# Kernel tuning notes

Hardware: AMD Instinct MI355X
Metric: run time of the kernel (lower is better)

Reference implementation:

```python
import jax, jax.numpy as jnp
import numpy as np

NUM_E = 100000
NUM_R = 500
HIDDEN = 64
BATCH = 32
GAMMA = 12.0
EPSILON = 2.0
EMB_RANGE = (GAMMA + EPSILON) / HIDDEN  # 0.21875
PI = 3.141592653589793


def setup_inputs() -> dict:
    key = jax.random.key(0)
    k1, k2, k3 = jax.random.split(key, 3)
    facts = jax.random.randint(k1, (BATCH, 3), 0, 1000, dtype=jnp.int64)  # col0<num_e, col1<2*num_r
    entity_embedding = jax.random.uniform(
        k2, (NUM_E, 2 * HIDDEN), dtype=jnp.float32, minval=-EMB_RANGE, maxval=EMB_RANGE)
    relation_embedding = jax.random.uniform(
        k3, (NUM_R * 2, HIDDEN), dtype=jnp.float32, minval=-EMB_RANGE, maxval=EMB_RANGE)
    return {"facts": facts, "entity_embedding": entity_embedding,
            "relation_embedding": relation_embedding}


def reference(facts, entity_embedding, relation_embedding):
    # Gather head/relation embeddings for the batch
    head = entity_embedding[facts[:, 0]]          # [B, 2D]
    relation = relation_embedding[facts[:, 1]]    # [B, D]

    re_head, im_head = jnp.split(head, 2, axis=1)           # [B, D] each
    re_tail, im_tail = jnp.split(entity_embedding, 2, axis=1)  # [E, D] each

    phase = relation / (EMB_RANGE / PI)
    re_rel = jnp.cos(phase)
    im_rel = jnp.sin(phase)

    # Complex rotation of head by relation: [B, D]
    re_rot = re_head * re_rel - im_head * im_rel
    im_rot = re_head * im_rel + im_head * re_rel

    # Broadcast difference against all entities: [B, E, D]
    re_diff = re_rot[:, None, :] - re_tail[None, :, :]
    im_diff = im_rot[:, None, :] - im_tail[None, :, :]

    # Per-component complex modulus, summed over dim -> [B, E]
    dist = jnp.sqrt(re_diff * re_diff + im_diff * im_diff).sum(axis=2)
    return GAMMA - dist
```

## Files before the change

kernel.cpp:

```cpp
#include <hip/hip_runtime.h>
#include <math.h>

#define NUM_E   100000
#define GAMMA_F 12.0f
#define EMB_RANGE_F 0.21875f
#define INV_TWO_EMB (1.0f / (2.0f * EMB_RANGE_F))

#define TILE_E  16
#define NT      (NUM_E / TILE_E)
#define GRID    2048

typedef float v4f __attribute__((ext_vector_type(4)));
typedef float v2f __attribute__((ext_vector_type(2)));

static __device__ __forceinline__ v2f pk_sub(v2f a, v2f b) {
    v2f d;
    asm("v_pk_add_f32 %0, %1, %2 neg_lo:[0,1] neg_hi:[0,1]"
        : "=v"(d) : "v"(a), "v"(b));
    return d;
}
static __device__ __forceinline__ v2f pk_mul(v2f a, v2f b) {
    v2f d;
    asm("v_pk_mul_f32 %0, %1, %2" : "=v"(d) : "v"(a), "v"(b));
    return d;
}
static __device__ __forceinline__ v2f pk_fma(v2f a, v2f b, v2f c) {
    v2f d;
    asm("v_pk_fma_f32 %0, %1, %2, %3" : "=v"(d) : "v"(a), "v"(b), "v"(c));
    return d;
}
static __device__ __forceinline__ float sq2(v2f dx, v2f dy) {
    v2f sq = pk_fma(dy, dy, pk_mul(dx, dx));
    return __builtin_amdgcn_sqrtf(sq.x) + __builtin_amdgcn_sqrtf(sq.y);
}
static __device__ __forceinline__ v2f lo2(v4f v) { return __builtin_shufflevector(v, v, 0, 1); }
static __device__ __forceinline__ v2f hi2(v4f v) { return __builtin_shufflevector(v, v, 2, 3); }

template <int CTRL>
static __device__ __forceinline__ float dpp_xor_add(float x) {
    int y = __builtin_amdgcn_update_dpp(0, __float_as_int(x), CTRL, 0xF, 0xF, true);
    return x + __int_as_float(y);
}

static __device__ __forceinline__ float dist_entity(
        v4f er0, v4f er1, v4f ei0, v4f ei1,
        const v2f RR[4], const v2f RI[4]) {
    v2f e2[4] = { lo2(er0), hi2(er0), lo2(er1), hi2(er1) };
    v2f i2[4] = { lo2(ei0), hi2(ei0), lo2(ei1), hi2(ei1) };
    float s0 = sq2(pk_sub(RR[0], e2[0]), pk_sub(RI[0], i2[0]));
    float s1 = sq2(pk_sub(RR[1], e2[1]), pk_sub(RI[1], i2[1]));
    float s2 = sq2(pk_sub(RR[2], e2[2]), pk_sub(RI[2], i2[2]));
    float s3 = sq2(pk_sub(RR[3], e2[3]), pk_sub(RI[3], i2[3]));
    float v = (s0 + s1) + (s2 + s3);
    v = dpp_xor_add<0xB1>(v);
    v = dpp_xor_add<0x4E>(v);
    v = dpp_xor_add<0x141>(v);
    return GAMMA_F - v;
}

static __device__ __forceinline__ void stage_chunk(const float* g, float* l) {
    __builtin_amdgcn_global_load_lds(
        (const __attribute__((address_space(1))) void*)g,
        (__attribute__((address_space(3))) void*)l,
        16, 0, 0);
}

__global__ __launch_bounds__(256, 2) void rotate_dist_fused(
        const int*   __restrict__ facts,
        const float* __restrict__ ent,
        const float* __restrict__ rel,
        float*       __restrict__ out) {
    __shared__ __align__(16) float sbuf[2][TILE_E * 128];

    const int t    = threadIdx.x;
    const int lane = t & 63;
    const int wv   = t >> 6;
    const int bq   = lane >> 3;
    const int dg   = lane & 7;
    const int b    = wv * 8 + bq;

    int tile = blockIdx.x;

    {
        const float* g = ent + (size_t)tile * (TILE_E * 128) + wv * 512 + lane * 4;
        float* l = &sbuf[0][wv * 512];
        stage_chunk(g, l);
        stage_chunk(g + 256, l + 256);
    }

    v2f RR[4], RI[4];
    {
        const int f0 = facts[b * 3 + 0];
        const int f1 = facts[b * 3 + 1];
        const float* hp = ent + (size_t)f0 * 128 + dg * 8;
        const float* rp = rel + (size_t)f1 * 64  + dg * 8;
        v4f hre0 = *(const v4f*)(hp);
        v4f hre1 = *(const v4f*)(hp + 4);
        v4f him0 = *(const v4f*)(hp + 64);
        v4f him1 = *(const v4f*)(hp + 68);
        v4f ph0  = *(const v4f*)(rp);
        v4f ph1  = *(const v4f*)(rp + 4);
        v4f rr0, rr1, ri0, ri1;
#pragma unroll
        for (int j = 0; j < 4; ++j) {
            float rev0 = ph0[j] * INV_TWO_EMB;
            float s0 = __builtin_amdgcn_sinf(rev0);
            float c0 = __builtin_amdgcn_cosf(rev0);
            rr0[j] = hre0[j] * c0 - him0[j] * s0;
            ri0[j] = hre0[j] * s0 + him0[j] * c0;
            float rev1 = ph1[j] * INV_TWO_EMB;
            float s1 = __builtin_amdgcn_sinf(rev1);
            float c1 = __builtin_amdgcn_cosf(rev1);
            rr1[j] = hre1[j] * c1 - him1[j] * s1;
            ri1[j] = hre1[j] * s1 + him1[j] * c1;
        }
        RR[0] = lo2(rr0); RR[1] = hi2(rr0); RR[2] = lo2(rr1); RR[3] = hi2(rr1);
        RI[0] = lo2(ri0); RI[1] = hi2(ri0); RI[2] = lo2(ri1); RI[3] = hi2(ri1);
    }

    float* obase = out + (size_t)b * NUM_E;

    int cur = 0;
    __syncthreads();

    while (true) {
        const int nxt = tile + GRID;
        if (nxt < NT) {
            const float* g = ent + (size_t)nxt * (TILE_E * 128) + wv * 512 + lane * 4;
            float* l = &sbuf[cur ^ 1][wv * 512];
            stage_chunk(g, l);
            stage_chunk(g + 256, l + 256);
        }

        const float* csrc = &sbuf[cur][0];
        float* op = obase + tile * TILE_E;
#pragma unroll
        for (int q = 0; q < 4; ++q) {
            v4f vout;
#pragma unroll
            for (int i = 0; i < 4; ++i) {
                const float* ep = csrc + (q * 4 + i) * 128 + dg * 8;
                v4f er0 = *(const v4f*)(ep);
                v4f er1 = *(const v4f*)(ep + 4);
                v4f ei0 = *(const v4f*)(ep + 64);
                v4f ei1 = *(const v4f*)(ep + 68);
                vout[i] = dist_entity(er0, er1, ei0, ei1, RR, RI);
            }
            if (dg == q) *(v4f*)(op + q * 4) = vout;
        }

        if (nxt >= NT) break;
        __syncthreads();
        cur ^= 1;
        tile = nxt;
    }
}

extern "C" void kernel_launch(void* const* d_in, const int* in_sizes, int n_in,
                              void* d_out, int out_size, void* d_ws, size_t ws_size,
                              hipStream_t stream) {
    const int*   facts = (const int*)d_in[0];
    const float* ent   = (const float*)d_in[1];
    const float* rel   = (const float*)d_in[2];
    float*       out   = (float*)d_out;
    (void)d_ws; (void)ws_size;

    rotate_dist_fused<<<dim3(GRID), dim3(256), 0, stream>>>(facts, ent, rel, out);
}
```

Baseline: 116.5 us.

## Compute two batch rows per thread to reuse each LDS entity load

Each wave now handles 16 batch rows on half of the entity tile instead of 8 rows on the whole tile. Each thread keeps rotated head vectors for two batch rows and reuses every entity value it reads from LDS for both of them, which halves LDS read traffic per distance. The cost is more registers per thread for the second set of rotated vectors, and the two DPP reductions are interleaved to hide their latency. Stores are split so different lanes write the two output rows.

```diff
diff --git a/kernel.cpp b/kernel.cpp
--- a/kernel.cpp
+++ b/kernel.cpp
@@ -42,27 +42,42 @@
     return x + __int_as_float(y);
 }
 
-static __device__ __forceinline__ float dist_entity(
-        v4f er0, v4f er1, v4f ei0, v4f ei1,
-        const v2f RR[4], const v2f RI[4]) {
-    v2f e2[4] = { lo2(er0), hi2(er0), lo2(er1), hi2(er1) };
-    v2f i2[4] = { lo2(ei0), hi2(ei0), lo2(ei1), hi2(ei1) };
-    float s0 = sq2(pk_sub(RR[0], e2[0]), pk_sub(RI[0], i2[0]));
-    float s1 = sq2(pk_sub(RR[1], e2[1]), pk_sub(RI[1], i2[1]));
-    float s2 = sq2(pk_sub(RR[2], e2[2]), pk_sub(RI[2], i2[2]));
-    float s3 = sq2(pk_sub(RR[3], e2[3]), pk_sub(RI[3], i2[3]));
-    float v = (s0 + s1) + (s2 + s3);
-    v = dpp_xor_add<0xB1>(v);
-    v = dpp_xor_add<0x4E>(v);
-    v = dpp_xor_add<0x141>(v);
-    return GAMMA_F - v;
-}
-
 static __device__ __forceinline__ void stage_chunk(const float* g, float* l) {
     __builtin_amdgcn_global_load_lds(
         (const __attribute__((address_space(1))) void*)g,
         (__attribute__((address_space(3))) void*)l,
         16, 0, 0);
+}
+
+static __device__ __forceinline__ void make_rot(
+        const int* __restrict__ facts, const float* __restrict__ ent,
+        const float* __restrict__ rel, int b, int dg, v2f RR[4], v2f RI[4]) {
+    const int f0 = facts[b * 3 + 0];
+    const int f1 = facts[b * 3 + 1];
+    const float* hp = ent + (size_t)f0 * 128 + dg * 8;
+    const float* rp = rel + (size_t)f1 * 64  + dg * 8;
+    v4f hre0 = *(const v4f*)(hp);
+    v4f hre1 = *(const v4f*)(hp + 4);
+    v4f him0 = *(const v4f*)(hp + 64);
+    v4f him1 = *(const v4f*)(hp + 68);
+    v4f ph0  = *(const v4f*)(rp);
+    v4f ph1  = *(const v4f*)(rp + 4);
+    v4f rr0, rr1, ri0, ri1;
+#pragma unroll
+    for (int j = 0; j < 4; ++j) {
+        float rev0 = ph0[j] * INV_TWO_EMB;
+        float s0 = __builtin_amdgcn_sinf(rev0);
+        float c0 = __builtin_amdgcn_cosf(rev0);
+        rr0[j] = hre0[j] * c0 - him0[j] * s0;
+        ri0[j] = hre0[j] * s0 + him0[j] * c0;
+        float rev1 = ph1[j] * INV_TWO_EMB;
+        float s1 = __builtin_amdgcn_sinf(rev1);
+        float c1 = __builtin_amdgcn_cosf(rev1);
+        rr1[j] = hre1[j] * c1 - him1[j] * s1;
+        ri1[j] = hre1[j] * s1 + him1[j] * c1;
+    }
+    RR[0] = lo2(rr0); RR[1] = hi2(rr0); RR[2] = lo2(rr1); RR[3] = hi2(rr1);
+    RI[0] = lo2(ri0); RI[1] = hi2(ri0); RI[2] = lo2(ri1); RI[3] = hi2(ri1);
 }
 
 __global__ __launch_bounds__(256, 2) void rotate_dist_fused(
@@ -77,7 +92,10 @@
     const int wv   = t >> 6;
     const int bq   = lane >> 3;
     const int dg   = lane & 7;
-    const int b    = wv * 8 + bq;
+    const int eh   = wv & 1;
+    const int bh   = wv >> 1;
+    const int b0   = bh * 16 + bq;
+    const int b1   = b0 + 8;
 
     int tile = blockIdx.x;
 
@@ -88,37 +106,12 @@
         stage_chunk(g + 256, l + 256);
     }
 
-    v2f RR[4], RI[4];
-    {
-        const int f0 = facts[b * 3 + 0];
-        const int f1 = facts[b * 3 + 1];
-        const float* hp = ent + (size_t)f0 * 128 + dg * 8;
-        const float* rp = rel + (size_t)f1 * 64  + dg * 8;
-        v4f hre0 = *(const v4f*)(hp);
-        v4f hre1 = *(const v4f*)(hp + 4);
-        v4f him0 = *(const v4f*)(hp + 64);
-        v4f him1 = *(const v4f*)(hp + 68);
-        v4f ph0  = *(const v4f*)(rp);
-        v4f ph1  = *(const v4f*)(rp + 4);
-        v4f rr0, rr1, ri0, ri1;
-#pragma unroll
-        for (int j = 0; j < 4; ++j) {
-            float rev0 = ph0[j] * INV_TWO_EMB;
-            float s0 = __builtin_amdgcn_sinf(rev0);
-            float c0 = __builtin_amdgcn_cosf(rev0);
-            rr0[j] = hre0[j] * c0 - him0[j] * s0;
-            ri0[j] = hre0[j] * s0 + him0[j] * c0;
-            float rev1 = ph1[j] * INV_TWO_EMB;
-            float s1 = __builtin_amdgcn_sinf(rev1);
-            float c1 = __builtin_amdgcn_cosf(rev1);
-            rr1[j] = hre1[j] * c1 - him1[j] * s1;
-            ri1[j] = hre1[j] * s1 + him1[j] * c1;
-        }
-        RR[0] = lo2(rr0); RR[1] = hi2(rr0); RR[2] = lo2(rr1); RR[3] = hi2(rr1);
-        RI[0] = lo2(ri0); RI[1] = hi2(ri0); RI[2] = lo2(ri1); RI[3] = hi2(ri1);
-    }
+    v2f RR0[4], RI0[4], RR1[4], RI1[4];
+    make_rot(facts, ent, rel, b0, dg, RR0, RI0);
+    make_rot(facts, ent, rel, b1, dg, RR1, RI1);
 
-    float* obase = out + (size_t)b * NUM_E;
+    float* orow0 = out + (size_t)b0 * NUM_E;
+    float* orow1 = out + (size_t)b1 * NUM_E;
 
     int cur = 0;
     __syncthreads();
@@ -132,21 +125,37 @@
             stage_chunk(g + 256, l + 256);
         }
 
-        const float* csrc = &sbuf[cur][0];
-        float* op = obase + tile * TILE_E;
+        const float* csrc = &sbuf[cur][0] + eh * (8 * 128) + dg * 8;
+        const int ebase = tile * TILE_E + eh * 8;
+
 #pragma unroll
-        for (int q = 0; q < 4; ++q) {
-            v4f vout;
+        for (int q = 0; q < 2; ++q) {
+            v4f vout0, vout1;
 #pragma unroll
             for (int i = 0; i < 4; ++i) {
-                const float* ep = csrc + (q * 4 + i) * 128 + dg * 8;
+                const float* ep = csrc + (q * 4 + i) * 128;
                 v4f er0 = *(const v4f*)(ep);
                 v4f er1 = *(const v4f*)(ep + 4);
                 v4f ei0 = *(const v4f*)(ep + 64);
                 v4f ei1 = *(const v4f*)(ep + 68);
-                vout[i] = dist_entity(er0, er1, ei0, ei1, RR, RI);
+                v2f e2[4] = { lo2(er0), hi2(er0), lo2(er1), hi2(er1) };
+                v2f i2[4] = { lo2(ei0), hi2(ei0), lo2(ei1), hi2(ei1) };
+                float v0 = (sq2(pk_sub(RR0[0], e2[0]), pk_sub(RI0[0], i2[0]))
+                          + sq2(pk_sub(RR0[1], e2[1]), pk_sub(RI0[1], i2[1])))
+                         + (sq2(pk_sub(RR0[2], e2[2]), pk_sub(RI0[2], i2[2]))
+                          + sq2(pk_sub(RR0[3], e2[3]), pk_sub(RI0[3], i2[3])));
+                float v1 = (sq2(pk_sub(RR1[0], e2[0]), pk_sub(RI1[0], i2[0]))
+                          + sq2(pk_sub(RR1[1], e2[1]), pk_sub(RI1[1], i2[1])))
+                         + (sq2(pk_sub(RR1[2], e2[2]), pk_sub(RI1[2], i2[2]))
+                          + sq2(pk_sub(RR1[3], e2[3]), pk_sub(RI1[3], i2[3])));
+                v0 = dpp_xor_add<0xB1>(v0);  v1 = dpp_xor_add<0xB1>(v1);
+                v0 = dpp_xor_add<0x4E>(v0);  v1 = dpp_xor_add<0x4E>(v1);
+                v0 = dpp_xor_add<0x141>(v0); v1 = dpp_xor_add<0x141>(v1);
+                vout0[i] = GAMMA_F - v0;
+                vout1[i] = GAMMA_F - v1;
             }
-            if (dg == q) *(v4f*)(op + q * 4) = vout;
+            if (dg == q)     *(v4f*)(orow0 + ebase + q * 4) = vout0;
+            if (dg == q + 4) *(v4f*)(orow1 + ebase + q * 4) = vout1;
         }
 
         if (nxt >= NT) break;
```

Result: no change. 116.4 us (-0.1%).

## Give each wave a private LDS ring and replace block barriers with vmcnt waits

Applied to the files above, without the earlier changes.

Each wave now stages its own copy of an 8-entity tile into a private double-buffered LDS slot. It waits with s_waitcnt vmcnt(0) instead of calling __syncthreads, which removes cross-wave barrier stalls in the streaming loop. The tile size drops from 16 to 8 entities and the grid shrinks from 2048 to 1280 blocks. In exchange, all four waves in a block issue the same global-to-LDS loads, so L2 traffic for the entity table is four times higher and more LDS is used. The head-rotation setup is moved into a helper function without changing what it computes.

```diff
diff --git a/kernel.cpp b/kernel.cpp
--- a/kernel.cpp
+++ b/kernel.cpp
@@ -6,9 +6,9 @@
 #define EMB_RANGE_F 0.21875f
 #define INV_TWO_EMB (1.0f / (2.0f * EMB_RANGE_F))
 
-#define TILE_E  16
-#define NT      (NUM_E / TILE_E)
-#define GRID    2048
+#define TILE_E  8
+#define NTIL    (NUM_E / TILE_E)
+#define GRIDB   1280
 
 typedef float v4f __attribute__((ext_vector_type(4)));
 typedef float v2f __attribute__((ext_vector_type(2)));
@@ -65,12 +65,43 @@
         16, 0, 0);
 }
 
+static __device__ __forceinline__ void make_rot(
+        const int* __restrict__ facts, const float* __restrict__ ent,
+        const float* __restrict__ rel, int b, int dg, v2f RR[4], v2f RI[4]) {
+    const int f0 = facts[b * 3 + 0];
+    const int f1 = facts[b * 3 + 1];
+    const float* hp = ent + (size_t)f0 * 128 + dg * 8;
+    const float* rp = rel + (size_t)f1 * 64  + dg * 8;
+    v4f hre0 = *(const v4f*)(hp);
+    v4f hre1 = *(const v4f*)(hp + 4);
+    v4f him0 = *(const v4f*)(hp + 64);
+    v4f him1 = *(const v4f*)(hp + 68);
+    v4f ph0  = *(const v4f*)(rp);
+    v4f ph1  = *(const v4f*)(rp + 4);
+    v4f rr0, rr1, ri0, ri1;
+#pragma unroll
+    for (int j = 0; j < 4; ++j) {
+        float rev0 = ph0[j] * INV_TWO_EMB;
+        float s0 = __builtin_amdgcn_sinf(rev0);
+        float c0 = __builtin_amdgcn_cosf(rev0);
+        rr0[j] = hre0[j] * c0 - him0[j] * s0;
+        ri0[j] = hre0[j] * s0 + him0[j] * c0;
+        float rev1 = ph1[j] * INV_TWO_EMB;
+        float s1 = __builtin_amdgcn_sinf(rev1);
+        float c1 = __builtin_amdgcn_cosf(rev1);
+        rr1[j] = hre1[j] * c1 - him1[j] * s1;
+        ri1[j] = hre1[j] * s1 + him1[j] * c1;
+    }
+    RR[0] = lo2(rr0); RR[1] = hi2(rr0); RR[2] = lo2(rr1); RR[3] = hi2(rr1);
+    RI[0] = lo2(ri0); RI[1] = hi2(ri0); RI[2] = lo2(ri1); RI[3] = hi2(ri1);
+}
+
 __global__ __launch_bounds__(256, 2) void rotate_dist_fused(
         const int*   __restrict__ facts,
         const float* __restrict__ ent,
         const float* __restrict__ rel,
         float*       __restrict__ out) {
-    __shared__ __align__(16) float sbuf[2][TILE_E * 128];
+    __shared__ __align__(16) float sbuf[4][2][TILE_E * 128];
 
     const int t    = threadIdx.x;
     const int lane = t & 63;
@@ -82,75 +113,51 @@
     int tile = blockIdx.x;
 
     {
-        const float* g = ent + (size_t)tile * (TILE_E * 128) + wv * 512 + lane * 4;
-        float* l = &sbuf[0][wv * 512];
-        stage_chunk(g, l);
-        stage_chunk(g + 256, l + 256);
+        const float* g = ent + (size_t)tile * (TILE_E * 128) + lane * 4;
+        float* l = &sbuf[wv][0][0];
+#pragma unroll
+        for (int c = 0; c < 4; ++c) stage_chunk(g + c * 256, l + c * 256);
     }
+    __builtin_amdgcn_sched_barrier(0);
 
     v2f RR[4], RI[4];
-    {
-        const int f0 = facts[b * 3 + 0];
-        const int f1 = facts[b * 3 + 1];
-        const float* hp = ent + (size_t)f0 * 128 + dg * 8;
-        const float* rp = rel + (size_t)f1 * 64  + dg * 8;
-        v4f hre0 = *(const v4f*)(hp);
-        v4f hre1 = *(const v4f*)(hp + 4);
-        v4f him0 = *(const v4f*)(hp + 64);
-        v4f him1 = *(const v4f*)(hp + 68);
-        v4f ph0  = *(const v4f*)(rp);
-        v4f ph1  = *(const v4f*)(rp + 4);
-        v4f rr0, rr1, ri0, ri1;
-#pragma unroll
-        for (int j = 0; j < 4; ++j) {
-            float rev0 = ph0[j] * INV_TWO_EMB;
-            float s0 = __builtin_amdgcn_sinf(rev0);
-            float c0 = __builtin_amdgcn_cosf(rev0);
-            rr0[j] = hre0[j] * c0 - him0[j] * s0;
-            ri0[j] = hre0[j] * s0 + him0[j] * c0;
-            float rev1 = ph1[j] * INV_TWO_EMB;
-            float s1 = __builtin_amdgcn_sinf(rev1);
-            float c1 = __builtin_amdgcn_cosf(rev1);
-            rr1[j] = hre1[j] * c1 - him1[j] * s1;
-            ri1[j] = hre1[j] * s1 + him1[j] * c1;
-        }
-        RR[0] = lo2(rr0); RR[1] = hi2(rr0); RR[2] = lo2(rr1); RR[3] = hi2(rr1);
-        RI[0] = lo2(ri0); RI[1] = hi2(ri0); RI[2] = lo2(ri1); RI[3] = hi2(ri1);
-    }
+    make_rot(facts, ent, rel, b, dg, RR, RI);
 
-    float* obase = out + (size_t)b * NUM_E;
+    float* orow = out + (size_t)b * NUM_E;
+
+    asm volatile("s_waitcnt vmcnt(0)" ::: "memory");
+    __builtin_amdgcn_sched_barrier(0);
 
     int cur = 0;
-    __syncthreads();
+    while (true) {
+        const int nxt = tile + GRIDB;
+        if (nxt < NTIL) {
+            const float* g = ent + (size_t)nxt * (TILE_E * 128) + lane * 4;
+            float* l = &sbuf[wv][cur ^ 1][0];
+#pragma unroll
+            for (int c = 0; c < 4; ++c) stage_chunk(g + c * 256, l + c * 256);
+        }
+        __builtin_amdgcn_sched_barrier(0);
 
-    while (true) {
-        const int nxt = tile + GRID;
-        if (nxt < NT) {
-            const float* g = ent + (size_t)nxt * (TILE_E * 128) + wv * 512 + lane * 4;
-            float* l = &sbuf[cur ^ 1][wv * 512];
-            stage_chunk(g, l);
-            stage_chunk(g + 256, l + 256);
+        const float* csrc = &sbuf[wv][cur][0] + dg * 8;
+        const int e0 = tile * TILE_E;
+        v4f vout0, vout1;
+#pragma unroll
+        for (int i = 0; i < 8; ++i) {
+            const float* ep = csrc + i * 128;
+            v4f er0 = *(const v4f*)(ep);
+            v4f er1 = *(const v4f*)(ep + 4);
+            v4f ei0 = *(const v4f*)(ep + 64);
+            v4f ei1 = *(const v4f*)(ep + 68);
+            float r = dist_entity(er0, er1, ei0, ei1, RR, RI);
+            if (i < 4) vout0[i] = r; else vout1[i - 4] = r;
         }
+        if (dg == 0) *(v4f*)(orow + e0)     = vout0;
+        if (dg == 1) *(v4f*)(orow + e0 + 4) = vout1;
 
-        const float* csrc = &sbuf[cur][0];
-        float* op = obase + tile * TILE_E;
-#pragma unroll
-        for (int q = 0; q < 4; ++q) {
-            v4f vout;
-#pragma unroll
-            for (int i = 0; i < 4; ++i) {
-                const float* ep = csrc + (q * 4 + i) * 128 + dg * 8;
-                v4f er0 = *(const v4f*)(ep);
-                v4f er1 = *(const v4f*)(ep + 4);
-                v4f ei0 = *(const v4f*)(ep + 64);
-                v4f ei1 = *(const v4f*)(ep + 68);
-                vout[i] = dist_entity(er0, er1, ei0, ei1, RR, RI);
-            }
-            if (dg == q) *(v4f*)(op + q * 4) = vout;
-        }
-
-        if (nxt >= NT) break;
-        __syncthreads();
+        if (nxt >= NTIL) break;
+        asm volatile("s_waitcnt vmcnt(0)" ::: "memory");
+        __builtin_amdgcn_sched_barrier(0);
         cur ^= 1;
         tile = nxt;
     }
@@ -165,5 +172,5 @@
     float*       out   = (float*)d_out;
     (void)d_ws; (void)ws_size;
 
-    rotate_dist_fused<<<dim3(GRID), dim3(256), 0, stream>>>(facts, ent, rel, out);
+    rotate_dist_fused<<<dim3(GRIDB), dim3(256), 0, stream>>>(facts, ent, rel, out);
 }
```

New measurement: 120.3 us. 3.3% more time.
